# Optimization experiments

Measured on AMD Instinct MI355X. Metric: run time of the kernel, lower is better.

## Reference

```python
import jax, jax.numpy as jnp
import numpy as np

WS = 7           # window side
N = WS * WS      # tokens per window = 49
DIM = 384
H = 12
HD = DIM // H    # 32
BW = 2048        # num_windows * batch
NW = 4           # windows per image (mask batch)
SCALE = 1.0 / float(np.sqrt(HD))


def _rel_index():
    coords = np.stack(np.meshgrid(np.arange(WS), np.arange(WS), indexing='ij'))  # (2,7,7)
    flat = coords.reshape(2, -1)                      # (2,49)
    rel = flat[:, :, None] - flat[:, None, :]         # (2,49,49)
    rel = rel.transpose(1, 2, 0).copy()               # (49,49,2)
    rel[..., 0] += WS - 1
    rel[..., 1] += WS - 1
    rel[..., 0] *= 2 * WS - 1
    return jnp.asarray(rel.sum(-1), dtype=jnp.int32)  # (49,49)


def setup_inputs() -> dict:
    key = jax.random.key(0)
    ks = jax.random.split(key, 16)
    f32 = jnp.float32
    se = jax.random.normal(ks[0], (BW, N, DIM), dtype=f32)
    de = jax.random.normal(ks[1], (BW, N, DIM), dtype=f32)
    mask = jnp.where(jax.random.uniform(ks[2], (NW, N, N)) < 0.1, f32(-1e9), f32(0.0))
    s = 0.02
    w_v_se = jax.random.normal(ks[3], (DIM, DIM), dtype=f32) * s
    b_v_se = jnp.zeros((DIM,), dtype=f32)
    w_qkv = jax.random.normal(ks[4], (3 * DIM, DIM), dtype=f32) * s
    b_qkv = jnp.zeros((3 * DIM,), dtype=f32)
    w_proj_se = jax.random.normal(ks[5], (DIM, DIM), dtype=f32) * s
    b_proj_se = jnp.zeros((DIM,), dtype=f32)
    w_proj_de = jax.random.normal(ks[6], (DIM, DIM), dtype=f32) * s
    b_proj_de = jnp.zeros((DIM,), dtype=f32)
    rpb = jax.random.normal(ks[7], ((2 * WS - 1) ** 2, H), dtype=f32) * s  # (169,12)
    rel_idx = _rel_index()
    return {
        'se': se, 'de': de, 'mask': mask,
        'w_v_se': w_v_se, 'b_v_se': b_v_se,
        'w_qkv': w_qkv, 'b_qkv': b_qkv,
        'w_proj_se': w_proj_se, 'b_proj_se': b_proj_se,
        'w_proj_de': w_proj_de, 'b_proj_de': b_proj_de,
        'rpb': rpb, 'rel_idx': rel_idx,
    }


def reference(se, de, mask, w_v_se, b_v_se, w_qkv, b_qkv,
              w_proj_se, b_proj_se, w_proj_de, b_proj_de, rpb, rel_idx):
    B_, N_, C = se.shape
    # qkv from de (coa=False branch)
    qkv = (de @ w_qkv.T + b_qkv).reshape(B_, N_, 3, H, HD).transpose(2, 0, 3, 1, 4)
    q, k, v_de = qkv[0], qkv[1], qkv[2]                 # (B_,H,N,HD)
    v_se = (se @ w_v_se.T + b_v_se).reshape(B_, N_, H, HD).transpose(0, 2, 1, 3)
    attn = jnp.einsum('bhnd,bhmd->bhnm', q * SCALE, k)  # (B_,H,N,N)
    bias = rpb[rel_idx].transpose(2, 0, 1)              # (H,N,N)
    attn = attn + bias[None]
    # add window mask: view as (B, nW, H, N, N)
    attn = attn.reshape(B_ // NW, NW, H, N_, N_) + mask[None, :, None]
    attn = jax.nn.softmax(attn.reshape(B_, H, N_, N_), axis=-1)
    se_o = jnp.einsum('bhnm,bhmd->bnhd', attn, v_se).reshape(B_, N_, C)
    de_o = jnp.einsum('bhnm,bhmd->bnhd', attn, v_de).reshape(B_, N_, C)
    se_o = se_o @ w_proj_se.T + b_proj_se
    de_o = de_o @ w_proj_de.T + b_proj_de
    return (se_o, de_o)
```

## Files before the change

### kernel.cpp

```cpp
#include <hip/hip_runtime.h>

typedef _Float16 f16;
typedef __attribute__((ext_vector_type(8))) _Float16 f16x8;
typedef __attribute__((ext_vector_type(4))) _Float16 f16x4;
typedef __attribute__((ext_vector_type(4))) float f32x4;

#define MFMA16(a, b, c) __builtin_amdgcn_mfma_f32_16x16x32_f16(a, b, c, 0, 0, 0)

#define SCALE_F 0.17677669529663687f
#define NHEAD 12
#define NTOK 49
#define NBW 2048

__global__ void cast_f32_to_f16(const float* __restrict__ in, f16* __restrict__ out, int n4) {
    int i0 = blockIdx.x * 256 + threadIdx.x;
    int stride = gridDim.x * 256;
    for (int i = i0; i < n4; i += stride) {
        f32x4 v = ((const f32x4*)in)[i];
        f16x4 o;
#pragma unroll
        for (int e = 0; e < 4; ++e) o[e] = (f16)v[e];
        ((f16x4*)out)[i] = o;
    }
}

__global__ void prep_bm(const float* __restrict__ rpb, const int* __restrict__ rel_idx,
                        const float* __restrict__ mask, float* __restrict__ bm) {
    int blk = blockIdx.x;
    int w4 = blk / NHEAD, h = blk - w4 * NHEAD;
    for (int idx = threadIdx.x; idx < 4096; idx += 64) {
        int r = idx >> 6, c = idx & 63;
        float v = -1e30f;
        if (r < NTOK && c < NTOK)
            v = rpb[rel_idx[r * NTOK + c] * NHEAD + h] + mask[(w4 * NTOK + r) * NTOK + c];
        bm[(size_t)blk * 4096 + idx] = v;
    }
}

template <typename OUT_T, bool A_F32>
__global__ __launch_bounds__(256) void gemm_bt(const void* __restrict__ Av, const f16* __restrict__ B,
                                               const float* __restrict__ bias, OUT_T* __restrict__ C,
                                               int M, int N, int K) {
    __shared__ __align__(16) f16 As[128 * 64];
    __shared__ __align__(16) f16 Bs[128 * 64];
    const int nwg = gridDim.x * gridDim.y;
    int wg = blockIdx.y * gridDim.x + blockIdx.x;
    wg = (wg & 7) * (nwg >> 3) + (wg >> 3);
    const int m0 = (wg / gridDim.x) * 128, n0 = (wg % gridDim.x) * 128;
    const int tid = threadIdx.x;
    const int w = tid >> 6, l = tid & 63;
    const int wm = w >> 1, wn = w & 1;
    const int lr = l & 15, lg = l >> 4;
    const int sp = l & 7;

    f32x4 acc[4][4] = {};

    for (int k0 = 0; k0 < K; k0 += 64) {
        __syncthreads();
        if constexpr (A_F32) {
            const float* A32 = (const float*)Av;
            f32x4 t0[4], t1[4];
#pragma unroll
            for (int it = 0; it < 4; ++it) {
                int row = w * 32 + it * 8 + (l >> 3);
                const float* g = A32 + (size_t)(m0 + row) * K + k0 + sp * 8;
                t0[it] = *(const f32x4*)g;
                t1[it] = *(const f32x4*)(g + 4);
            }
#pragma unroll
            for (int it = 0; it < 4; ++it) {
                int row = w * 32 + it * 8 + (l >> 3);
                f16x8 hx;
#pragma unroll
                for (int e = 0; e < 4; ++e) {
                    hx[e] = (f16)t0[it][e];
                    hx[e + 4] = (f16)t1[it][e];
                }
                *(f16x8*)(As + row * 64 + (sp ^ (row & 7)) * 8) = hx;
            }
#pragma unroll
            for (int it = 0; it < 4; ++it) {
                int row = w * 32 + it * 8 + (l >> 3);
                int gchunk = sp ^ (row & 7);
                const f16* gB = B + (size_t)(n0 + row) * K + k0 + gchunk * 8;
                f16* lB = Bs + (w * 32 + it * 8) * 64;
                __builtin_amdgcn_global_load_lds((const __attribute__((address_space(1))) void*)gB,
                                                 (__attribute__((address_space(3))) void*)lB, 16, 0, 0);
            }
        } else {
            const f16* A16 = (const f16*)Av;
#pragma unroll
            for (int it = 0; it < 4; ++it) {
                int row = w * 32 + it * 8 + (l >> 3);
                int gchunk = sp ^ (row & 7);
                const f16* gA = A16 + (size_t)(m0 + row) * K + k0 + gchunk * 8;
                const f16* gB = B + (size_t)(n0 + row) * K + k0 + gchunk * 8;
                f16* lA = As + (w * 32 + it * 8) * 64;
                f16* lB = Bs + (w * 32 + it * 8) * 64;
                __builtin_amdgcn_global_load_lds((const __attribute__((address_space(1))) void*)gA,
                                                 (__attribute__((address_space(3))) void*)lA, 16, 0, 0);
                __builtin_amdgcn_global_load_lds((const __attribute__((address_space(1))) void*)gB,
                                                 (__attribute__((address_space(3))) void*)lB, 16, 0, 0);
            }
        }
        __syncthreads();
#pragma unroll
        for (int ks = 0; ks < 2; ++ks) {
            f16x8 af[4], bfr[4];
#pragma unroll
            for (int mi = 0; mi < 4; ++mi) {
                int r = 64 * wm + 16 * mi + lr;
                int chunk = (lg + 4 * ks) ^ (r & 7);
                af[mi] = *(const f16x8*)(As + r * 64 + chunk * 8);
            }
#pragma unroll
            for (int ni = 0; ni < 4; ++ni) {
                int r = 64 * wn + 16 * ni + lr;
                int chunk = (lg + 4 * ks) ^ (r & 7);
                bfr[ni] = *(const f16x8*)(Bs + r * 64 + chunk * 8);
            }
#pragma unroll
            for (int mi = 0; mi < 4; ++mi)
#pragma unroll
                for (int ni = 0; ni < 4; ++ni)
                    acc[mi][ni] = MFMA16(af[mi], bfr[ni], acc[mi][ni]);
        }
    }
#pragma unroll
    for (int mi = 0; mi < 4; ++mi) {
#pragma unroll
        for (int ni = 0; ni < 4; ++ni) {
            int col = n0 + 64 * wn + 16 * ni + lr;
            float bv = bias[col];
#pragma unroll
            for (int reg = 0; reg < 4; ++reg) {
                int row = m0 + 64 * wm + 16 * mi + 4 * lg + reg;
                C[(size_t)row * N + col] = (OUT_T)(acc[mi][ni][reg] + bv);
            }
        }
    }
}

__global__ __launch_bounds__(64) void attn_kernel(const f16* __restrict__ qkv,
                                                  const f16* __restrict__ vse,
                                                  const float* __restrict__ bm_all,
                                                  f16* __restrict__ att_se, f16* __restrict__ att_de) {
    __shared__ __align__(16) f16 Ps[64 * 64];

    const int bh = blockIdx.x;
    const int b = bh / NHEAD, h = bh - b * NHEAD;
    const int l = threadIdx.x;
    const int lr = l & 15, lg = l >> 4;
    const size_t wbase = (size_t)b * NTOK;

    f16x8 qa[4], kb[4];
#pragma unroll
    for (int mi = 0; mi < 4; ++mi)
        qa[mi] = *(const f16x8*)(qkv + (wbase + 16 * mi + lr) * 1152 + h * 32 + lg * 8);
#pragma unroll
    for (int ni = 0; ni < 4; ++ni)
        kb[ni] = *(const f16x8*)(qkv + (wbase + 16 * ni + lr) * 1152 + 384 + h * 32 + lg * 8);

    const f32x4 zero4 = {0.f, 0.f, 0.f, 0.f};
    f32x4 S[4][4];
    __builtin_amdgcn_s_setprio(1);
#pragma unroll
    for (int mi = 0; mi < 4; ++mi)
#pragma unroll
        for (int ni = 0; ni < 4; ++ni)
            S[mi][ni] = MFMA16(qa[mi], kb[ni], zero4);
    __builtin_amdgcn_s_setprio(0);

    f16x8 vbr[2][2][2];
#pragma unroll
    for (int s = 0; s < 2; ++s) {
        const f16* vbase = s ? (qkv + wbase * 1152 + 768 + h * 32) : (vse + wbase * 384 + h * 32);
        const int RS = s ? 1152 : 384;
#pragma unroll
        for (int ks = 0; ks < 2; ++ks)
#pragma unroll
            for (int ni = 0; ni < 2; ++ni) {
                const f16* p = vbase + (size_t)(8 * lg + 32 * ks) * RS + 16 * ni + lr;
#pragma unroll
                for (int e = 0; e < 8; ++e) vbr[s][ks][ni][e] = p[(size_t)e * RS];
            }
    }

    const float* bmp = bm_all + (size_t)((b & 3) * NHEAD + h) * 4096;
#pragma unroll
    for (int mi = 0; mi < 4; ++mi) {
#pragma unroll
        for (int reg = 0; reg < 4; ++reg) {
            int r = 16 * mi + 4 * lg + reg;
            float v[4];
#pragma unroll
            for (int ni = 0; ni < 4; ++ni)
                v[ni] = S[mi][ni][reg] * SCALE_F + bmp[(r << 6) + 16 * ni + lr];
            float mx = fmaxf(fmaxf(v[0], v[1]), fmaxf(v[2], v[3]));
#pragma unroll
            for (int off = 1; off < 16; off <<= 1) mx = fmaxf(mx, __shfl_xor(mx, off));
            float e[4];
            float sm = 0.f;
#pragma unroll
            for (int ni = 0; ni < 4; ++ni) {
                e[ni] = __expf(v[ni] - mx);
                sm += e[ni];
            }
#pragma unroll
            for (int off = 1; off < 16; off <<= 1) sm += __shfl_xor(sm, off);
            float inv = 1.f / sm;
#pragma unroll
            for (int ni = 0; ni < 4; ++ni)
                Ps[(r << 6) + ((16 * ni + lr) ^ ((r & 7) << 3))] = (f16)(e[ni] * inv);
        }
    }
    __syncthreads();

#pragma unroll
    for (int s = 0; s < 2; ++s) {
        f32x4 o[4][2] = {};
#pragma unroll
        for (int ks = 0; ks < 2; ++ks) {
            f16x8 pa[4];
#pragma unroll
            for (int mi = 0; mi < 4; ++mi) {
                int r = 16 * mi + lr;
                pa[mi] = *(const f16x8*)(Ps + (r << 6) + ((8 * lg + 32 * ks) ^ ((r & 7) << 3)));
            }
            __builtin_amdgcn_s_setprio(1);
#pragma unroll
            for (int ni = 0; ni < 2; ++ni)
#pragma unroll
                for (int mi = 0; mi < 4; ++mi) o[mi][ni] = MFMA16(pa[mi], vbr[s][ks][ni], o[mi][ni]);
            __builtin_amdgcn_s_setprio(0);
        }
        f16* dst = s ? att_de : att_se;
#pragma unroll
        for (int mi = 0; mi < 4; ++mi) {
#pragma unroll
            for (int reg = 0; reg < 4; ++reg) {
                int r = 16 * mi + 4 * lg + reg;
                if (r < NTOK) {
#pragma unroll
                    for (int ni = 0; ni < 2; ++ni)
                        dst[(wbase + r) * 384 + h * 32 + 16 * ni + lr] = (f16)o[mi][ni][reg];
                }
            }
        }
    }
}

extern "C" void kernel_launch(void* const* d_in, const int* in_sizes, int n_in,
                              void* d_out, int out_size, void* d_ws, size_t ws_size,
                              hipStream_t stream) {
    const float* se = (const float*)d_in[0];
    const float* de = (const float*)d_in[1];
    const float* mask = (const float*)d_in[2];
    const float* w_v_se = (const float*)d_in[3];
    const float* b_v_se = (const float*)d_in[4];
    const float* w_qkv = (const float*)d_in[5];
    const float* b_qkv = (const float*)d_in[6];
    const float* w_proj_se = (const float*)d_in[7];
    const float* b_proj_se = (const float*)d_in[8];
    const float* w_proj_de = (const float*)d_in[9];
    const float* b_proj_de = (const float*)d_in[10];
    const float* rpb = (const float*)d_in[11];
    const int* rel_idx = (const int*)d_in[12];

    const size_t SE_ELEMS = (size_t)NBW * NTOK * 384;

    char* ws = (char*)d_ws;
    f16* att_se = (f16*)(ws);
    f16* att_de = (f16*)(ws + 77070336);
    f16* qkv_h = (f16*)(ws + 154140672);
    f16* vse_h = (f16*)(ws + 385351680);
    f16* wqkv_h = (f16*)(ws + 462422016);
    f16* wvse_h = (f16*)(ws + 463306752);
    f16* wpse_h = (f16*)(ws + 463601664);
    f16* wpde_h = (f16*)(ws + 463896576);
    float* bm = (float*)(ws + 464191488);

    auto cast = [&](const float* in, f16* out, size_t n) {
        int n4 = (int)(n / 4);
        int blocks = (n4 + 255) / 256;
        if (blocks > 2048) blocks = 2048;
        cast_f32_to_f16<<<blocks, 256, 0, stream>>>(in, out, n4);
    };
    cast(w_qkv, wqkv_h, (size_t)1152 * 384);
    cast(w_v_se, wvse_h, (size_t)384 * 384);
    cast(w_proj_se, wpse_h, (size_t)384 * 384);
    cast(w_proj_de, wpde_h, (size_t)384 * 384);

    prep_bm<<<48, 64, 0, stream>>>(rpb, rel_idx, mask, bm);

    gemm_bt<f16, true><<<dim3(9, 784), 256, 0, stream>>>((const void*)de, wqkv_h, b_qkv, qkv_h, 100352, 1152, 384);
    gemm_bt<f16, true><<<dim3(3, 784), 256, 0, stream>>>((const void*)se, wvse_h, b_v_se, vse_h, 100352, 384, 384);

    attn_kernel<<<NBW * NHEAD, 64, 0, stream>>>(qkv_h, vse_h, bm, att_se, att_de);

    gemm_bt<float, false><<<dim3(3, 784), 256, 0, stream>>>((const void*)att_se, wpse_h, b_proj_se, (float*)d_out,
                                                            100352, 384, 384);
    gemm_bt<float, false><<<dim3(3, 784), 256, 0, stream>>>((const void*)att_de, wpde_h, b_proj_de,
                                                            (float*)d_out + SE_ELEMS, 100352, 384, 384);
}
```

Baseline: 613.8 us.

## Pipeline GEMM loads, emit transposed V, pack two heads per attention block

The GEMM main loop is restructured into a software pipeline: the next A tile is loaded into registers while the current one is converted and written to LDS, with explicit waitcnt and barrier control and raised priority around the MFMAs. The QKV and V-projection epilogues now write V in a per-head transposed layout padded to 56 tokens, and fold the softmax scale into Q. This lets the attention kernel read V with vector loads instead of strided scalar loads. The attention kernel runs two heads per 128-thread block, each wave with its own LDS buffer, and replaces the block barrier with a wave-local wait. The four weight casts are merged into one launch. The scattered transposed stores in the epilogue and the hand-written wait counts add complexity and are a correctness risk.

```diff
diff --git a/kernel.cpp b/kernel.cpp
--- a/kernel.cpp
+++ b/kernel.cpp
@@ -11,17 +11,29 @@
 #define NHEAD 12
 #define NTOK 49
 #define NBW 2048
-
-__global__ void cast_f32_to_f16(const float* __restrict__ in, f16* __restrict__ out, int n4) {
-    int i0 = blockIdx.x * 256 + threadIdx.x;
-    int stride = gridDim.x * 256;
-    for (int i = i0; i < n4; i += stride) {
-        f32x4 v = ((const f32x4*)in)[i];
-        f16x4 o;
-#pragma unroll
-        for (int e = 0; e < 4; ++e) o[e] = (f16)v[e];
-        ((f16x4*)out)[i] = o;
-    }
+#define VTJ 56
+
+#define SB() __builtin_amdgcn_s_barrier()
+#define SCHEDB() __builtin_amdgcn_sched_barrier(0)
+#define WAITL0() asm volatile("s_waitcnt lgkmcnt(0)" ::: "memory")
+
+__global__ void cast_weights(const float* __restrict__ wqkv, const float* __restrict__ wvse,
+                             const float* __restrict__ wpse, const float* __restrict__ wpde,
+                             f16* o_qkv, f16* o_vse, f16* o_pse, f16* o_pde) {
+    int i = blockIdx.x * 256 + threadIdx.x;
+    if (i >= 221184) return;
+    const float* src;
+    f16* dst;
+    int off;
+    if (i < 110592) { src = wqkv; dst = o_qkv; off = i; }
+    else if (i < 147456) { src = wvse; dst = o_vse; off = i - 110592; }
+    else if (i < 184320) { src = wpse; dst = o_pse; off = i - 147456; }
+    else { src = wpde; dst = o_pde; off = i - 184320; }
+    f32x4 v = ((const f32x4*)src)[off];
+    f16x4 o;
+#pragma unroll
+    for (int e = 0; e < 4; ++e) o[e] = (f16)v[e];
+    ((f16x4*)dst)[off] = o;
 }
 
 __global__ void prep_bm(const float* __restrict__ rpb, const int* __restrict__ rel_idx,
@@ -37,10 +49,10 @@
     }
 }
 
-template <typename OUT_T, bool A_F32>
+template <int EPI, bool A_F32, typename OUT_T>
 __global__ __launch_bounds__(256) void gemm_bt(const void* __restrict__ Av, const f16* __restrict__ B,
                                                const float* __restrict__ bias, OUT_T* __restrict__ C,
-                                               int M, int N, int K) {
+                                               f16* __restrict__ VT, int N, int ldc) {
     __shared__ __align__(16) f16 As[128 * 64];
     __shared__ __align__(16) f16 Bs[128 * 64];
     const int nwg = gridDim.x * gridDim.y;
@@ -52,58 +64,69 @@
     const int wm = w >> 1, wn = w & 1;
     const int lr = l & 15, lg = l >> 4;
     const int sp = l & 7;
+    const int lrow = l >> 3;
 
     f32x4 acc[4][4] = {};
-
-    for (int k0 = 0; k0 < K; k0 += 64) {
-        __syncthreads();
-        if constexpr (A_F32) {
-            const float* A32 = (const float*)Av;
-            f32x4 t0[4], t1[4];
-#pragma unroll
-            for (int it = 0; it < 4; ++it) {
-                int row = w * 32 + it * 8 + (l >> 3);
-                const float* g = A32 + (size_t)(m0 + row) * K + k0 + sp * 8;
+    f32x4 t0[4], t1[4];
+    f16x8 tf[4];
+
+    auto LOADA = [&](int kt) {
+#pragma unroll
+        for (int it = 0; it < 4; ++it) {
+            int row = w * 32 + it * 8 + lrow;
+            if constexpr (A_F32) {
+                const float* g = (const float*)Av + (size_t)(m0 + row) * 384 + kt * 64 + sp * 8;
                 t0[it] = *(const f32x4*)g;
                 t1[it] = *(const f32x4*)(g + 4);
-            }
-#pragma unroll
-            for (int it = 0; it < 4; ++it) {
-                int row = w * 32 + it * 8 + (l >> 3);
-                f16x8 hx;
-#pragma unroll
-                for (int e = 0; e < 4; ++e) {
-                    hx[e] = (f16)t0[it][e];
-                    hx[e + 4] = (f16)t1[it][e];
-                }
-                *(f16x8*)(As + row * 64 + (sp ^ (row & 7)) * 8) = hx;
-            }
-#pragma unroll
-            for (int it = 0; it < 4; ++it) {
-                int row = w * 32 + it * 8 + (l >> 3);
-                int gchunk = sp ^ (row & 7);
-                const f16* gB = B + (size_t)(n0 + row) * K + k0 + gchunk * 8;
-                f16* lB = Bs + (w * 32 + it * 8) * 64;
-                __builtin_amdgcn_global_load_lds((const __attribute__((address_space(1))) void*)gB,
-                                                 (__attribute__((address_space(3))) void*)lB, 16, 0, 0);
-            }
+            } else {
+                tf[it] = *(const f16x8*)((const f16*)Av + (size_t)(m0 + row) * 384 + kt * 64 + sp * 8);
+            }
+        }
+    };
+    auto CVTWRITE = [&]() {
+#pragma unroll
+        for (int it = 0; it < 4; ++it) {
+            int row = w * 32 + it * 8 + lrow;
+            f16x8 hx;
+            if constexpr (A_F32) {
+#pragma unroll
+                for (int e = 0; e < 4; ++e) { hx[e] = (f16)t0[it][e]; hx[e + 4] = (f16)t1[it][e]; }
+            } else {
+                hx = tf[it];
+            }
+            *(f16x8*)(As + row * 64 + (sp ^ (row & 7)) * 8) = hx;
+        }
+    };
+    auto STAGEB = [&](int kt) {
+#pragma unroll
+        for (int it = 0; it < 4; ++it) {
+            int row = w * 32 + it * 8 + lrow;
+            int gchunk = sp ^ (row & 7);
+            const f16* gB = B + (size_t)(n0 + row) * 384 + kt * 64 + gchunk * 8;
+            f16* lB = Bs + (w * 32 + it * 8) * 64;
+            __builtin_amdgcn_global_load_lds((const __attribute__((address_space(1))) void*)gB,
+                                             (__attribute__((address_space(3))) void*)lB, 16, 0, 0);
+        }
+    };
+
+    LOADA(0);
+#pragma unroll
+    for (int t = 0; t < 6; ++t) {
+        WAITL0();
+        SB();
+        SCHEDB();
+        CVTWRITE();
+        STAGEB(t);
+        if (t < 5) LOADA(t + 1);
+        WAITL0();
+        if (t < 5) {
+            if constexpr (A_F32) asm volatile("s_waitcnt vmcnt(8)" ::: "memory");
+            else asm volatile("s_waitcnt vmcnt(4)" ::: "memory");
         } else {
-            const f16* A16 = (const f16*)Av;
-#pragma unroll
-            for (int it = 0; it < 4; ++it) {
-                int row = w * 32 + it * 8 + (l >> 3);
-                int gchunk = sp ^ (row & 7);
-                const f16* gA = A16 + (size_t)(m0 + row) * K + k0 + gchunk * 8;
-                const f16* gB = B + (size_t)(n0 + row) * K + k0 + gchunk * 8;
-                f16* lA = As + (w * 32 + it * 8) * 64;
-                f16* lB = Bs + (w * 32 + it * 8) * 64;
-                __builtin_amdgcn_global_load_lds((const __attribute__((address_space(1))) void*)gA,
-                                                 (__attribute__((address_space(3))) void*)lA, 16, 0, 0);
-                __builtin_amdgcn_global_load_lds((const __attribute__((address_space(1))) void*)gB,
-                                                 (__attribute__((address_space(3))) void*)lB, 16, 0, 0);
-            }
-        }
-        __syncthreads();
+            asm volatile("s_waitcnt vmcnt(0)" ::: "memory");
+        }
+        SB();
+        SCHEDB();
 #pragma unroll
         for (int ks = 0; ks < 2; ++ks) {
             f16x8 af[4], bfr[4];
@@ -119,13 +142,16 @@
                 int chunk = (lg + 4 * ks) ^ (r & 7);
                 bfr[ni] = *(const f16x8*)(Bs + r * 64 + chunk * 8);
             }
+            __builtin_amdgcn_s_setprio(1);
 #pragma unroll
             for (int mi = 0; mi < 4; ++mi)
 #pragma unroll
                 for (int ni = 0; ni < 4; ++ni)
                     acc[mi][ni] = MFMA16(af[mi], bfr[ni], acc[mi][ni]);
-        }
-    }
+            __builtin_amdgcn_s_setprio(0);
+        }
+    }
+
 #pragma unroll
     for (int mi = 0; mi < 4; ++mi) {
 #pragma unroll
@@ -135,31 +161,49 @@
 #pragma unroll
             for (int reg = 0; reg < 4; ++reg) {
                 int row = m0 + 64 * wm + 16 * mi + 4 * lg + reg;
-                C[(size_t)row * N + col] = (OUT_T)(acc[mi][ni][reg] + bv);
-            }
-        }
-    }
-}
-
-__global__ __launch_bounds__(64) void attn_kernel(const f16* __restrict__ qkv,
-                                                  const f16* __restrict__ vse,
-                                                  const float* __restrict__ bm_all,
-                                                  f16* __restrict__ att_se, f16* __restrict__ att_de) {
-    __shared__ __align__(16) f16 Ps[64 * 64];
-
-    const int bh = blockIdx.x;
+                float v = acc[mi][ni][reg] + bv;
+                if constexpr (EPI == 0) {
+                    C[(size_t)row * ldc + col] = (OUT_T)v;
+                } else if constexpr (EPI == 1) {
+                    if (col < 768) {
+                        if (col < 384) v *= SCALE_F;
+                        C[(size_t)row * 768 + col] = (OUT_T)v;
+                    } else {
+                        int c2 = col - 768;
+                        int b = row / 49, j = row - b * 49;
+                        VT[((size_t)b * NHEAD + (c2 >> 5)) * (32 * VTJ) + (c2 & 31) * VTJ + j] = (f16)v;
+                    }
+                } else {
+                    int b = row / 49, j = row - b * 49;
+                    VT[((size_t)b * NHEAD + (col >> 5)) * (32 * VTJ) + (col & 31) * VTJ + j] = (f16)v;
+                }
+            }
+        }
+    }
+}
+
+__global__ __launch_bounds__(128) void attn_kernel(const f16* __restrict__ qk,
+                                                   const f16* __restrict__ vse_t,
+                                                   const f16* __restrict__ vde_t,
+                                                   const float* __restrict__ bm_all,
+                                                   f16* __restrict__ att_se, f16* __restrict__ att_de) {
+    __shared__ __align__(16) f16 Ps[2][64 * 64];
+
+    const int wv = threadIdx.x >> 6;
+    const int l = threadIdx.x & 63;
+    const int bh = blockIdx.x * 2 + wv;
     const int b = bh / NHEAD, h = bh - b * NHEAD;
-    const int l = threadIdx.x;
     const int lr = l & 15, lg = l >> 4;
     const size_t wbase = (size_t)b * NTOK;
+    f16* P = Ps[wv];
 
     f16x8 qa[4], kb[4];
 #pragma unroll
     for (int mi = 0; mi < 4; ++mi)
-        qa[mi] = *(const f16x8*)(qkv + (wbase + 16 * mi + lr) * 1152 + h * 32 + lg * 8);
+        qa[mi] = *(const f16x8*)(qk + (wbase + 16 * mi + lr) * 768 + h * 32 + lg * 8);
 #pragma unroll
     for (int ni = 0; ni < 4; ++ni)
-        kb[ni] = *(const f16x8*)(qkv + (wbase + 16 * ni + lr) * 1152 + 384 + h * 32 + lg * 8);
+        kb[ni] = *(const f16x8*)(qk + (wbase + 16 * ni + lr) * 768 + 384 + h * 32 + lg * 8);
 
     const f32x4 zero4 = {0.f, 0.f, 0.f, 0.f};
     f32x4 S[4][4];
@@ -174,15 +218,14 @@
     f16x8 vbr[2][2][2];
 #pragma unroll
     for (int s = 0; s < 2; ++s) {
-        const f16* vbase = s ? (qkv + wbase * 1152 + 768 + h * 32) : (vse + wbase * 384 + h * 32);
-        const int RS = s ? 1152 : 384;
+        const f16* vt = (s ? vde_t : vse_t) + (size_t)bh * (32 * VTJ);
 #pragma unroll
         for (int ks = 0; ks < 2; ++ks)
 #pragma unroll
             for (int ni = 0; ni < 2; ++ni) {
-                const f16* p = vbase + (size_t)(8 * lg + 32 * ks) * RS + 16 * ni + lr;
-#pragma unroll
-                for (int e = 0; e < 8; ++e) vbr[s][ks][ni][e] = p[(size_t)e * RS];
+                int j0 = 8 * lg + 32 * ks;
+                if (j0 == 56) j0 = 48;
+                vbr[s][ks][ni] = *(const f16x8*)(vt + (16 * ni + lr) * VTJ + j0);
             }
     }
 
@@ -195,7 +238,7 @@
             float v[4];
 #pragma unroll
             for (int ni = 0; ni < 4; ++ni)
-                v[ni] = S[mi][ni][reg] * SCALE_F + bmp[(r << 6) + 16 * ni + lr];
+                v[ni] = S[mi][ni][reg] + bmp[(r << 6) + 16 * ni + lr];
             float mx = fmaxf(fmaxf(v[0], v[1]), fmaxf(v[2], v[3]));
 #pragma unroll
             for (int off = 1; off < 16; off <<= 1) mx = fmaxf(mx, __shfl_xor(mx, off));
@@ -211,10 +254,11 @@
             float inv = 1.f / sm;
 #pragma unroll
             for (int ni = 0; ni < 4; ++ni)
-                Ps[(r << 6) + ((16 * ni + lr) ^ ((r & 7) << 3))] = (f16)(e[ni] * inv);
-        }
-    }
-    __syncthreads();
+                P[(r << 6) + ((16 * ni + lr) ^ ((r & 7) << 3))] = (f16)(e[ni] * inv);
+        }
+    }
+    WAITL0();
+    SCHEDB();
 
 #pragma unroll
     for (int s = 0; s < 2; ++s) {
@@ -225,7 +269,7 @@
 #pragma unroll
             for (int mi = 0; mi < 4; ++mi) {
                 int r = 16 * mi + lr;
-                pa[mi] = *(const f16x8*)(Ps + (r << 6) + ((8 * lg + 32 * ks) ^ ((r & 7) << 3)));
+                pa[mi] = *(const f16x8*)(P + (r << 6) + ((8 * lg + 32 * ks) ^ ((r & 7) << 3)));
             }
             __builtin_amdgcn_s_setprio(1);
 #pragma unroll
@@ -272,34 +316,28 @@
     char* ws = (char*)d_ws;
     f16* att_se = (f16*)(ws);
     f16* att_de = (f16*)(ws + 77070336);
-    f16* qkv_h = (f16*)(ws + 154140672);
-    f16* vse_h = (f16*)(ws + 385351680);
-    f16* wqkv_h = (f16*)(ws + 462422016);
-    f16* wvse_h = (f16*)(ws + 463306752);
-    f16* wpse_h = (f16*)(ws + 463601664);
-    f16* wpde_h = (f16*)(ws + 463896576);
-    float* bm = (float*)(ws + 464191488);
-
-    auto cast = [&](const float* in, f16* out, size_t n) {
-        int n4 = (int)(n / 4);
-        int blocks = (n4 + 255) / 256;
-        if (blocks > 2048) blocks = 2048;
-        cast_f32_to_f16<<<blocks, 256, 0, stream>>>(in, out, n4);
-    };
-    cast(w_qkv, wqkv_h, (size_t)1152 * 384);
-    cast(w_v_se, wvse_h, (size_t)384 * 384);
-    cast(w_proj_se, wpse_h, (size_t)384 * 384);
-    cast(w_proj_de, wpde_h, (size_t)384 * 384);
-
+    f16* qk_h   = (f16*)(ws + 154140672);
+    f16* vse_t  = (f16*)(ws + 308281344);
+    f16* vde_t  = (f16*)(ws + 396361728);
+    f16* wqkv_h = (f16*)(ws + 484442112);
+    f16* wvse_h = (f16*)(ws + 485326848);
+    f16* wpse_h = (f16*)(ws + 485621760);
+    f16* wpde_h = (f16*)(ws + 485916672);
+    float* bm   = (float*)(ws + 486211584);
+
+    cast_weights<<<864, 256, 0, stream>>>(w_qkv, w_v_se, w_proj_se, w_proj_de,
+                                          wqkv_h, wvse_h, wpse_h, wpde_h);
     prep_bm<<<48, 64, 0, stream>>>(rpb, rel_idx, mask, bm);
 
-    gemm_bt<f16, true><<<dim3(9, 784), 256, 0, stream>>>((const void*)de, wqkv_h, b_qkv, qkv_h, 100352, 1152, 384);
-    gemm_bt<f16, true><<<dim3(3, 784), 256, 0, stream>>>((const void*)se, wvse_h, b_v_se, vse_h, 100352, 384, 384);
-
-    attn_kernel<<<NBW * NHEAD, 64, 0, stream>>>(qkv_h, vse_h, bm, att_se, att_de);
-
-    gemm_bt<float, false><<<dim3(3, 784), 256, 0, stream>>>((const void*)att_se, wpse_h, b_proj_se, (float*)d_out,
-                                                            100352, 384, 384);
-    gemm_bt<float, false><<<dim3(3, 784), 256, 0, stream>>>((const void*)att_de, wpde_h, b_proj_de,
-                                                            (float*)d_out + SE_ELEMS, 100352, 384, 384);
-}
+    gemm_bt<1, true, f16><<<dim3(9, 784), 256, 0, stream>>>((const void*)de, wqkv_h, b_qkv,
+                                                            qk_h, vde_t, 1152, 768);
+    gemm_bt<2, true, f16><<<dim3(3, 784), 256, 0, stream>>>((const void*)se, wvse_h, b_v_se,
+                                                            (f16*)nullptr, vse_t, 384, 384);
+
+    attn_kernel<<<NBW * NHEAD / 2, 128, 0, stream>>>(qk_h, vse_t, vde_t, bm, att_se, att_de);
+
+    gemm_bt<0, false, float><<<dim3(3, 784), 256, 0, stream>>>((const void*)att_se, wpse_h, b_proj_se,
+                                                               (float*)d_out, nullptr, 384, 384);
+    gemm_bt<0, false, float><<<dim3(3, 784), 256, 0, stream>>>((const void*)att_de, wpde_h, b_proj_de,
+                                                               (float*)d_out + SE_ELEMS, nullptr, 384, 384);
+}
```

After: 697.6 us. +13.7%, slower.

## Merge weight casts, pack two attention waves per block, prioritize GEMM MFMAs

Applied to the files above, without the earlier changes.

The four weight-cast launches become one kernel that covers all four weight tensors. The attention kernel now runs two independent waves per 128-thread block, each with its own shared-memory P tile. The block-wide barrier is replaced by an lgkmcnt wait plus a scheduling barrier, which is enough because each wave reads back only the tile it wrote. The GEMM inner loop also wraps its MFMA batch in s_setprio. Together these aim to cut launch overhead, reduce per-block scheduling cost in attention, and improve MFMA issue priority, with small gains expected from each.

```diff
diff --git a/kernel.cpp b/kernel.cpp
--- a/kernel.cpp
+++ b/kernel.cpp
@@ -12,16 +12,26 @@
 #define NTOK 49
 #define NBW 2048
 
-__global__ void cast_f32_to_f16(const float* __restrict__ in, f16* __restrict__ out, int n4) {
-    int i0 = blockIdx.x * 256 + threadIdx.x;
-    int stride = gridDim.x * 256;
-    for (int i = i0; i < n4; i += stride) {
-        f32x4 v = ((const f32x4*)in)[i];
-        f16x4 o;
-#pragma unroll
-        for (int e = 0; e < 4; ++e) o[e] = (f16)v[e];
-        ((f16x4*)out)[i] = o;
-    }
+#define SCHEDB() __builtin_amdgcn_sched_barrier(0)
+#define WAITL0() asm volatile("s_waitcnt lgkmcnt(0)" ::: "memory")
+
+__global__ void cast_weights(const float* __restrict__ wqkv, const float* __restrict__ wvse,
+                             const float* __restrict__ wpse, const float* __restrict__ wpde,
+                             f16* o_qkv, f16* o_vse, f16* o_pse, f16* o_pde) {
+    int i = blockIdx.x * 256 + threadIdx.x;
+    if (i >= 221184) return;
+    const float* src;
+    f16* dst;
+    int off;
+    if (i < 110592) { src = wqkv; dst = o_qkv; off = i; }
+    else if (i < 147456) { src = wvse; dst = o_vse; off = i - 110592; }
+    else if (i < 184320) { src = wpse; dst = o_pse; off = i - 147456; }
+    else { src = wpde; dst = o_pde; off = i - 184320; }
+    f32x4 v = ((const f32x4*)src)[off];
+    f16x4 o;
+#pragma unroll
+    for (int e = 0; e < 4; ++e) o[e] = (f16)v[e];
+    ((f16x4*)dst)[off] = o;
 }
 
 __global__ void prep_bm(const float* __restrict__ rpb, const int* __restrict__ rel_idx,
@@ -119,11 +129,13 @@
                 int chunk = (lg + 4 * ks) ^ (r & 7);
                 bfr[ni] = *(const f16x8*)(Bs + r * 64 + chunk * 8);
             }
+            __builtin_amdgcn_s_setprio(1);
 #pragma unroll
             for (int mi = 0; mi < 4; ++mi)
 #pragma unroll
                 for (int ni = 0; ni < 4; ++ni)
                     acc[mi][ni] = MFMA16(af[mi], bfr[ni], acc[mi][ni]);
+            __builtin_amdgcn_s_setprio(0);
         }
     }
 #pragma unroll
@@ -141,17 +153,19 @@
     }
 }
 
-__global__ __launch_bounds__(64) void attn_kernel(const f16* __restrict__ qkv,
-                                                  const f16* __restrict__ vse,
-                                                  const float* __restrict__ bm_all,
-                                                  f16* __restrict__ att_se, f16* __restrict__ att_de) {
-    __shared__ __align__(16) f16 Ps[64 * 64];
-
-    const int bh = blockIdx.x;
+__global__ __launch_bounds__(128) void attn_kernel(const f16* __restrict__ qkv,
+                                                   const f16* __restrict__ vse,
+                                                   const float* __restrict__ bm_all,
+                                                   f16* __restrict__ att_se, f16* __restrict__ att_de) {
+    __shared__ __align__(16) f16 Ps[2][64 * 64];
+
+    const int wv = threadIdx.x >> 6;
+    const int l = threadIdx.x & 63;
+    const int bh = blockIdx.x * 2 + wv;
     const int b = bh / NHEAD, h = bh - b * NHEAD;
-    const int l = threadIdx.x;
     const int lr = l & 15, lg = l >> 4;
     const size_t wbase = (size_t)b * NTOK;
+    f16* P = Ps[wv];
 
     f16x8 qa[4], kb[4];
 #pragma unroll
@@ -211,10 +225,11 @@
             float inv = 1.f / sm;
 #pragma unroll
             for (int ni = 0; ni < 4; ++ni)
-                Ps[(r << 6) + ((16 * ni + lr) ^ ((r & 7) << 3))] = (f16)(e[ni] * inv);
-        }
-    }
-    __syncthreads();
+                P[(r << 6) + ((16 * ni + lr) ^ ((r & 7) << 3))] = (f16)(e[ni] * inv);
+        }
+    }
+    WAITL0();
+    SCHEDB();
 
 #pragma unroll
     for (int s = 0; s < 2; ++s) {
@@ -225,7 +240,7 @@
 #pragma unroll
             for (int mi = 0; mi < 4; ++mi) {
                 int r = 16 * mi + lr;
-                pa[mi] = *(const f16x8*)(Ps + (r << 6) + ((8 * lg + 32 * ks) ^ ((r & 7) << 3)));
+                pa[mi] = *(const f16x8*)(P + (r << 6) + ((8 * lg + 32 * ks) ^ ((r & 7) << 3)));
             }
             __builtin_amdgcn_s_setprio(1);
 #pragma unroll
@@ -280,23 +295,14 @@
     f16* wpde_h = (f16*)(ws + 463896576);
     float* bm = (float*)(ws + 464191488);
 
-    auto cast = [&](const float* in, f16* out, size_t n) {
-        int n4 = (int)(n / 4);
-        int blocks = (n4 + 255) / 256;
-        if (blocks > 2048) blocks = 2048;
-        cast_f32_to_f16<<<blocks, 256, 0, stream>>>(in, out, n4);
-    };
-    cast(w_qkv, wqkv_h, (size_t)1152 * 384);
-    cast(w_v_se, wvse_h, (size_t)384 * 384);
-    cast(w_proj_se, wpse_h, (size_t)384 * 384);
-    cast(w_proj_de, wpde_h, (size_t)384 * 384);
-
+    cast_weights<<<864, 256, 0, stream>>>(w_qkv, w_v_se, w_proj_se, w_proj_de,
+                                          wqkv_h, wvse_h, wpse_h, wpde_h);
     prep_bm<<<48, 64, 0, stream>>>(rpb, rel_idx, mask, bm);
 
     gemm_bt<f16, true><<<dim3(9, 784), 256, 0, stream>>>((const void*)de, wqkv_h, b_qkv, qkv_h, 100352, 1152, 384);
     gemm_bt<f16, true><<<dim3(3, 784), 256, 0, stream>>>((const void*)se, wvse_h, b_v_se, vse_h, 100352, 384, 384);
 
-    attn_kernel<<<NBW * NHEAD, 64, 0, stream>>>(qkv_h, vse_h, bm, att_se, att_de);
+    attn_kernel<<<NBW * NHEAD / 2, 128, 0, stream>>>(qkv_h, vse_h, bm, att_se, att_de);
 
     gemm_bt<float, false><<<dim3(3, 784), 256, 0, stream>>>((const void*)att_se, wpse_h, b_proj_se, (float*)d_out,
                                                             100352, 384, 384);
```

New measurement: 644.2 us. 1.05x slower.
